# Kernel optimization log

Measured on AMD Instinct MI355X. Metric: run time of the kernel, lower is better.

The kernel has to match this reference:

```python
import jax, jax.numpy as jnp
import numpy as np
from jax import lax

# --- configuration (matches init_kwargs) ---
NY_I = NX_I = 256      # interior model size
PML = 20               # pml width on each edge
DX = 4.0               # grid spacing (m)
DT = 5e-4              # time step (s); CFL: vmax*DT/DX ~ 0.4 < 0.5
NT = 64                # number of time steps
C1, C2 = 9.0 / 8.0, -1.0 / 24.0   # 4th-order staggered FD coefficients


def _shift(p, axis, off, n):
    idx = [slice(None)] * 3
    idx[axis] = slice(2 + off, 2 + off + n)
    return p[tuple(idx)]


def _dfwd(f, axis):
    # forward (half-cell +) staggered derivative, 4th order, zero halo
    pad = [(0, 0)] * 3
    pad[axis] = (2, 2)
    p = jnp.pad(f, pad)
    n = f.shape[axis]
    return (C1 * (_shift(p, axis, 1, n) - _shift(p, axis, 0, n))
            + C2 * (_shift(p, axis, 2, n) - _shift(p, axis, -1, n))) / DX


def _dbwd(f, axis):
    # backward (half-cell -) staggered derivative, 4th order, zero halo
    pad = [(0, 0)] * 3
    pad[axis] = (2, 2)
    p = jnp.pad(f, pad)
    n = f.shape[axis]
    return (C1 * (_shift(p, axis, 0, n) - _shift(p, axis, -1, n))
            + C2 * (_shift(p, axis, 1, n) - _shift(p, axis, -2, n))) / DX


def _propagate(lamb, mu, buoyancy, amps, src_loc, rec_loc):
    # replicate model edges into the PML region (as deepwave does)
    lambp = jnp.pad(lamb, PML, mode='edge')[None]      # [1,NY,NX]
    mup = jnp.pad(mu, PML, mode='edge')[None]
    buoyp = jnp.pad(buoyancy, PML, mode='edge')[None]
    NY, NX = lambp.shape[1], lambp.shape[2]
    n_shots = amps.shape[0]
    l2m = lambp + 2.0 * mup

    # CPML damping profiles (quadratic), alpha=0, kappa=1
    max_vel = lax.stop_gradient(jnp.max(jnp.sqrt(l2m * buoyp)))
    sig_max = 3.0 * max_vel * jnp.log(1000.0) / (2.0 * PML * DX)

    def prof(n):
        i = jnp.arange(n, dtype=lamb.dtype)
        d = jnp.maximum(jnp.clip(PML - i, 0.0, None),
                        jnp.clip(i - (n - 1 - PML), 0.0, None)) / PML
        return sig_max * d * d

    by = jnp.exp(-prof(NY) * DT)[None, :, None]
    ay = by - 1.0
    bx = jnp.exp(-prof(NX) * DT)[None, None, :]
    ax = bx - 1.0

    shot = jnp.arange(n_shots)[:, None]
    sl = src_loc + PML   # [S,nsrc,2]
    rl = rec_loc + PML   # [S,nrec,2]
    src_b = buoyp[0, sl[..., 0], sl[..., 1]]   # buoyancy at sources [S,nsrc]

    z = jnp.zeros((n_shots, NY, NX), lamb.dtype)
    carry0 = (z,) * 13  # vy,vx,syy,sxy,sxx, m_vyy,m_vyx,m_vxy,m_vxx, m_syyy,m_sxyy,m_sxyx,m_sxxx

    def step(carry, amp_t):
        (vy, vx, syy, sxy, sxx,
         mvyy, mvyx, mvxy, mvxx,
         msyyy, msxyy, msxyx, msxxx) = carry
        # --- velocity update ---
        d = _dbwd(syy, 1); msyyy = by * msyyy + ay * d; dsyy_y = d + msyyy
        d = _dbwd(sxy, 2); msxyx = bx * msxyx + ax * d; dsxy_x = d + msxyx
        vy = vy + DT * buoyp * (dsyy_y + dsxy_x)
        d = _dbwd(sxy, 1); msxyy = by * msxyy + ay * d; dsxy_y = d + msxyy
        d = _dbwd(sxx, 2); msxxx = bx * msxxx + ax * d; dsxx_x = d + msxxx
        vx = vx + DT * buoyp * (dsxy_y + dsxx_x)
        # --- inject y-oriented sources into vy ---
        vy = vy.at[shot, sl[..., 0], sl[..., 1]].add(DT * src_b * amp_t)
        # --- stress update ---
        d = _dfwd(vy, 1); mvyy = by * mvyy + ay * d; dvy_y = d + mvyy
        d = _dfwd(vx, 2); mvxx = bx * mvxx + ax * d; dvx_x = d + mvxx
        syy = syy + DT * (l2m * dvy_y + lambp * dvx_x)
        sxx = sxx + DT * (lambp * dvy_y + l2m * dvx_x)
        d = _dfwd(vy, 2); mvyx = bx * mvyx + ax * d; dvy_x = d + mvyx
        d = _dfwd(vx, 1); mvxy = by * mvxy + ay * d; dvx_y = d + mvxy
        sxy = sxy + DT * mup * (dvy_x + dvx_y)
        # --- record y-oriented receivers ---
        rec = vy[shot, rl[..., 0], rl[..., 1]]   # [S,nrec]
        return ((vy, vx, syy, sxy, sxx,
                 mvyy, mvyx, mvxy, mvxx,
                 msyyy, msxyy, msxyx, msxxx), rec)

    _, recs = lax.scan(step, carry0, jnp.moveaxis(amps, 2, 0))  # recs [nt,S,nrec]
    return jnp.transpose(recs, (1, 2, 0))  # [S,nrec,nt]


def setup_inputs() -> dict:
    key = jax.random.key(0)
    k = jax.random.split(key, 6)
    vp = 3000.0 + 100.0 * jax.random.normal(k[0], (NY_I, NX_I), jnp.float32)
    vs = 1500.0 + 50.0 * jax.random.normal(k[1], (NY_I, NX_I), jnp.float32)
    rho = 2200.0 + 50.0 * jax.random.normal(k[2], (NY_I, NX_I), jnp.float32)
    mu = rho * vs ** 2
    lamb = rho * (vp ** 2 - 2.0 * vs ** 2)
    buoyancy = 1.0 / rho
    source_amplitudes_y = jax.random.normal(k[3], (2, 8, NT), jnp.float32)
    source_locations_y = jax.random.randint(k[4], (2, 8, 2), 0, NY_I)
    receiver_locations_y = jax.random.randint(k[5], (2, 64, 2), 0, NY_I)
    return {
        'lamb': lamb, 'mu': mu, 'buoyancy': buoyancy,
        'source_amplitudes_y': source_amplitudes_y,
        'source_locations_y': source_locations_y,
        'receiver_locations_y': receiver_locations_y,
    }


def reference(lamb, mu, buoyancy, source_amplitudes_y,
              source_locations_y, receiver_locations_y):
    return _propagate(lamb, mu, buoyancy, source_amplitudes_y,
                      source_locations_y, receiver_locations_y)
```

## Files before the change

### kernel.cpp

```cpp
#include <hip/hip_runtime.h>
#include <math.h>

static constexpr int NYI  = 256;
static constexpr int PMLW = 20;
static constexpr int NY   = 296, NX = 296;
static constexpr int NCELL = NY * NX;
static constexpr int NS   = 2;
static constexpr int NSRC = 8;
static constexpr int NREC = 64;
static constexpr int NT   = 64;
static constexpr float DXF = 4.0f;
static constexpr float DTF = 5e-4f;
static constexpr float FC1 = 9.0f / 8.0f;
static constexpr float FC2 = -1.0f / 24.0f;
static constexpr float INV_DX = 1.0f / DXF;

static constexpr int TB = 8, TS = 37;
static constexpr int VS = TS + 4;
static constexpr int SS = TS + 8;
static constexpr int NBLK = TB * TB * NS;
static constexpr int NTHR = 512;
static constexpr int VAREA = VS * VS;
static constexpr int TAREA = TS * TS;
static constexpr int SFRAME = SS * SS - TAREA;
static constexpr int KV = 4, KT = 3;

static constexpr int GSLOT   = 3 * NS * NCELL;
static constexpr int FLG_OFF = 2 * GSLOT;

__device__ __forceinline__ float cohload(const float* p) {
    return __hip_atomic_load(p, __ATOMIC_RELAXED, __HIP_MEMORY_SCOPE_AGENT);
}
__device__ __forceinline__ void cohstore(float* p, float v) {
    __hip_atomic_store(p, v, __ATOMIC_RELAXED, __HIP_MEMORY_SCOPE_AGENT);
}

__global__ __launch_bounds__(NTHR, 1)
void elastic_fused(const float* __restrict__ lamb, const float* __restrict__ mu,
                   const float* __restrict__ buoy, const float* __restrict__ amps,
                   const int* __restrict__ src_loc, const int* __restrict__ rec_loc,
                   float* __restrict__ out, float* __restrict__ ws)
{
    __shared__ float sS[3][SS * SS];
    __shared__ float sV[2][VS * VS];
    __shared__ float byt[VS], ayt[VS], bxt[VS], axt[VS];
    __shared__ float sAmp[NSRC * NT];
    __shared__ float wmax[NTHR / 64];
    __shared__ int   rcnt;
    __shared__ short rl_r[NREC];
    __shared__ int   rl_pos[NREC];

    int* flags = (int*)(ws + FLG_OFF);
    float* gstr = ws;

    const int tid  = threadIdx.x;
    const int shot = blockIdx.x & 1;
    const int tb   = blockIdx.x >> 1;
    const int bty  = tb >> 3, btx = tb & 7;
    const int gy0  = bty * TS, gx0 = btx * TS;
    const int myBlk = blockIdx.x;

    int myNbr = -1;
    if (tid < 8) {
        int idx = tid < 4 ? tid : tid + 1;
        int dy = idx / 3 - 1, dx = idx % 3 - 1;
        int nty = bty + dy, ntx = btx + dx;
        if (nty >= 0 && nty < TB && ntx >= 0 && ntx < TB)
            myNbr = ((nty * TB + ntx) << 1) | shot;
    }

    for (int i = tid; i < 3 * SS * SS; i += NTHR) ((float*)sS)[i] = 0.0f;
    for (int i = tid; i < 2 * VS * VS; i += NTHR) ((float*)sV)[i] = 0.0f;
    if (tid == 0) rcnt = 0;

    float vmax = 0.0f;
    for (int i = tid * 4; i < NYI * NYI; i += NTHR * 4) {
        const float4 la4 = *(const float4*)(lamb + i);
        const float4 mu4 = *(const float4*)(mu + i);
        const float4 b4  = *(const float4*)(buoy + i);
        vmax = fmaxf(vmax, (la4.x + 2.0f * mu4.x) * b4.x);
        vmax = fmaxf(vmax, (la4.y + 2.0f * mu4.y) * b4.y);
        vmax = fmaxf(vmax, (la4.z + 2.0f * mu4.z) * b4.z);
        vmax = fmaxf(vmax, (la4.w + 2.0f * mu4.w) * b4.w);
    }
    #pragma unroll
    for (int off = 32; off > 0; off >>= 1)
        vmax = fmaxf(vmax, __shfl_down(vmax, off));
    if ((tid & 63) == 0) wmax[tid >> 6] = vmax;

    int   sidx_v[KV], vyv[KV], vxv[KV], smk[KV];
    float buo_v[KV];
    float msyyy[KV] = {0,0,0,0}, msxyx[KV] = {0,0,0,0};
    float msxyy[KV] = {0,0,0,0}, msxxx[KV] = {0,0,0,0};
    unsigned cvm = 0, intm = 0;
    #pragma unroll
    for (int k = 0; k < KV; ++k) {
        int vi = tid + NTHR * k;
        bool val = vi < VAREA;
        int vy_ = val ? vi / VS : 0;
        int vx_ = val ? vi - vy_ * VS : 0;
        int gy = gy0 - 2 + vy_, gx = gx0 - 2 + vx_;
        bool ing = val && gy >= 0 && gy < NY && gx >= 0 && gx < NX;
        if (ing) cvm |= 1u << k;
        if (ing && vy_ >= 4 && vy_ <= 37 && vx_ >= 4 && vx_ <= 37) intm |= 1u << k;
        vyv[k] = vy_; vxv[k] = vx_;
        sidx_v[k] = (vy_ + 2) * SS + (vx_ + 2);
        float b = 0.0f;
        if (ing) {
            int iy = min(max(gy - PMLW, 0), NYI - 1);
            int ix = min(max(gx - PMLW, 0), NYI - 1);
            b = buoy[iy * NYI + ix];
        }
        buo_v[k] = b;
        int sm = 0;
        #pragma unroll
        for (int s = 0; s < NSRC; ++s) {
            int sy = src_loc[(shot * NSRC + s) * 2 + 0] + PMLW;
            int sx = src_loc[(shot * NSRC + s) * 2 + 1] + PMLW;
            if (ing && sy == gy && sx == gx) sm |= 1 << s;
        }
        smk[k] = sm;
    }
    const unsigned bndm = cvm & ~intm;

    int   sidx_t[KT], vidx_t[KT], gidx_t[KT], tyt[KT], txt[KT];
    float lam_t[KT], mu_t[KT], l2m_t[KT];
    float mvyy[KT] = {0,0,0}, mvxx[KT] = {0,0,0}, mvyx[KT] = {0,0,0}, mvxy[KT] = {0,0,0};
    unsigned ctm = 0, ringm = 0;
    #pragma unroll
    for (int k = 0; k < KT; ++k) {
        int ti = tid + NTHR * k;
        bool val = ti < TAREA;
        int ty = val ? ti / TS : 0;
        int tx = val ? ti - ty * TS : 0;
        int gy = gy0 + ty, gx = gx0 + tx;
        if (val) ctm |= 1u << k;
        if (val && (ty < 4 || ty >= TS - 4 || tx < 4 || tx >= TS - 4)) ringm |= 1u << k;
        tyt[k] = ty; txt[k] = tx;
        sidx_t[k] = (ty + 4) * SS + (tx + 4);
        vidx_t[k] = (ty + 2) * VS + (tx + 2);
        gidx_t[k] = gy * NX + gx;
        float la = 0.0f, m = 0.0f;
        if (val) {
            int iy = min(max(gy - PMLW, 0), NYI - 1);
            int ix = min(max(gx - PMLW, 0), NYI - 1);
            la = lamb[iy * NYI + ix];
            m  = mu  [iy * NYI + ix];
        }
        lam_t[k] = la; mu_t[k] = m; l2m_t[k] = la + 2.0f * m;
    }

    bool fval[2], fin[2];
    int  flidx[2], fgi[2];
    #pragma unroll
    for (int k = 0; k < 2; ++k) {
        int ff = tid + NTHR * k;
        fval[k] = ff < SFRAME;
        int fy = 0, fx = 0;
        if (fval[k]) {
            if (ff < 4 * SS)      { fy = ff / SS;                 fx = ff - fy * SS; }
            else if (ff < 8 * SS) { int r = ff - 4 * SS; fy = SS - 4 + r / SS; fx = r % SS; }
            else {
                int r = ff - 8 * SS;
                if (r < (SS - 8) * 4) { fy = 4 + (r >> 2); fx = r & 3; }
                else { r -= (SS - 8) * 4; fy = 4 + (r >> 2); fx = SS - 4 + (r & 3); }
            }
        }
        int gy = gy0 - 4 + fy, gx = gx0 - 4 + fx;
        fin[k]   = fval[k] && gy >= 0 && gy < NY && gx >= 0 && gx < NX;
        flidx[k] = fy * SS + fx;
        fgi[k]   = fin[k] ? (gy * NX + gx) : 0;
    }

    __syncthreads();

    float vall = wmax[0];
    #pragma unroll
    for (int w = 1; w < NTHR / 64; ++w) vall = fmaxf(vall, wmax[w]);
    const float max_vel = sqrtf(vall);
    const float sig_max = 3.0f * max_vel * logf(1000.0f) / (2.0f * PMLW * DXF);
    if (tid < VS) {
        auto prof = [&](int g) -> float {
            float fi = (float)g;
            float d1 = fmaxf((float)PMLW - fi, 0.0f);
            float d2 = fmaxf(fi - (float)(NY - 1 - PMLW), 0.0f);
            float dd = fmaxf(d1, d2) * (1.0f / (float)PMLW);
            return expf(-(sig_max * dd * dd) * DTF);
        };
        float b = prof(gy0 - 2 + tid); byt[tid] = b; ayt[tid] = b - 1.0f;
        b = prof(gx0 - 2 + tid);       bxt[tid] = b; axt[tid] = b - 1.0f;
    }
    if (tid < NREC) {
        int r = tid;
        int ry = rec_loc[(shot * NREC + r) * 2 + 0] + PMLW;
        int rx = rec_loc[(shot * NREC + r) * 2 + 1] + PMLW;
        if (ry >= gy0 && ry < gy0 + TS && rx >= gx0 && rx < gx0 + TS) {
            int p = atomicAdd(&rcnt, 1);
            rl_r[p]   = (short)r;
            rl_pos[p] = (ry - gy0 + 2) * VS + (rx - gx0 + 2);
        }
    }
    for (int i = tid; i < NSRC * NT; i += NTHR)
        sAmp[i] = amps[shot * NSRC * NT + i];
    __syncthreads();

    auto do_vel = [&](unsigned m, int t) {
        #pragma unroll
        for (int k = 0; k < KV; ++k) {
            if (!((m >> k) & 1)) continue;
            int si = sidx_v[k];
            float by_ = byt[vyv[k]], ay_ = ayt[vyv[k]];
            float bx_ = bxt[vxv[k]], ax_ = axt[vxv[k]];
            float d, mm;
            d = (FC1 * (sS[0][si] - sS[0][si - SS]) + FC2 * (sS[0][si + SS] - sS[0][si - 2 * SS])) * INV_DX;
            mm = by_ * msyyy[k] + ay_ * d;  msyyy[k] = mm;  float dsyy_y = d + mm;
            d = (FC1 * (sS[1][si] - sS[1][si - 1]) + FC2 * (sS[1][si + 1] - sS[1][si - 2])) * INV_DX;
            mm = bx_ * msxyx[k] + ax_ * d;  msxyx[k] = mm;  float dsxy_x = d + mm;
            d = (FC1 * (sS[1][si] - sS[1][si - SS]) + FC2 * (sS[1][si + SS] - sS[1][si - 2 * SS])) * INV_DX;
            mm = by_ * msxyy[k] + ay_ * d;  msxyy[k] = mm;  float dsxy_y = d + mm;
            d = (FC1 * (sS[2][si] - sS[2][si - 1]) + FC2 * (sS[2][si + 1] - sS[2][si - 2])) * INV_DX;
            mm = bx_ * msxxx[k] + ax_ * d;  msxxx[k] = mm;  float dsxx_x = d + mm;
            int vi = tid + NTHR * k;
            float nvy = sV[0][vi] + DTF * buo_v[k] * (dsyy_y + dsxy_x);
            float nvx = sV[1][vi] + DTF * buo_v[k] * (dsxy_y + dsxx_x);
            if (smk[k]) {
                #pragma unroll
                for (int s = 0; s < NSRC; ++s)
                    if ((smk[k] >> s) & 1) nvy += DTF * buo_v[k] * sAmp[s * NT + t];
            }
            sV[0][vi] = nvy;
            sV[1][vi] = nvx;
        }
    };

    for (int t = 0; t < NT; ++t) {
        const float* gsr = gstr + ((t + 1) & 1) * GSLOT;
        float*       gsw = gstr + (t & 1) * GSLOT;

        do_vel(intm, t);

        if (t > 0 && myNbr >= 0) {
            while (__hip_atomic_load(&flags[myNbr], __ATOMIC_RELAXED,
                                     __HIP_MEMORY_SCOPE_AGENT) < t)
                __builtin_amdgcn_s_sleep(1);
        }
        __syncthreads();

        float fr0[3], fr1[3];
        #pragma unroll
        for (int f = 0; f < 3; ++f) {
            fr0[f] = (t > 0 && fin[0]) ? cohload(&gsr[(f * NS + shot) * NCELL + fgi[0]]) : 0.0f;
            fr1[f] = (t > 0 && fin[1]) ? cohload(&gsr[(f * NS + shot) * NCELL + fgi[1]]) : 0.0f;
        }
        if (fval[0]) { sS[0][flidx[0]] = fr0[0]; sS[1][flidx[0]] = fr0[1]; sS[2][flidx[0]] = fr0[2]; }
        if (fval[1]) { sS[0][flidx[1]] = fr1[0]; sS[1][flidx[1]] = fr1[1]; sS[2][flidx[1]] = fr1[2]; }
        __syncthreads();

        do_vel(bndm, t);
        __syncthreads();

        if (tid < rcnt)
            out[(shot * NREC + rl_r[tid]) * NT + t] = sV[0][rl_pos[tid]];

        #pragma unroll
        for (int k = 0; k < KT; ++k) {
            if (!((ctm >> k) & 1)) continue;
            int si = sidx_t[k], vi = vidx_t[k];
            float by_ = byt[tyt[k] + 2], ay_ = ayt[tyt[k] + 2];
            float bx_ = bxt[txt[k] + 2], ax_ = axt[txt[k] + 2];
            float d, mm;
            d = (FC1 * (sV[0][vi + VS] - sV[0][vi]) + FC2 * (sV[0][vi + 2 * VS] - sV[0][vi - VS])) * INV_DX;
            mm = by_ * mvyy[k] + ay_ * d;  mvyy[k] = mm;  float dvy_y = d + mm;
            d = (FC1 * (sV[1][vi + 1] - sV[1][vi]) + FC2 * (sV[1][vi + 2] - sV[1][vi - 1])) * INV_DX;
            mm = bx_ * mvxx[k] + ax_ * d;  mvxx[k] = mm;  float dvx_x = d + mm;
            float nsyy = sS[0][si] + DTF * (l2m_t[k] * dvy_y + lam_t[k] * dvx_x);
            float nsxx = sS[2][si] + DTF * (lam_t[k] * dvy_y + l2m_t[k] * dvx_x);
            d = (FC1 * (sV[0][vi + 1] - sV[0][vi]) + FC2 * (sV[0][vi + 2] - sV[0][vi - 1])) * INV_DX;
            mm = bx_ * mvyx[k] + ax_ * d;  mvyx[k] = mm;  float dvy_x = d + mm;
            d = (FC1 * (sV[1][vi + VS] - sV[1][vi]) + FC2 * (sV[1][vi + 2 * VS] - sV[1][vi - VS])) * INV_DX;
            mm = by_ * mvxy[k] + ay_ * d;  mvxy[k] = mm;  float dvx_y = d + mm;
            float nsxy = sS[1][si] + DTF * mu_t[k] * (dvy_x + dvx_y);
            sS[0][si] = nsyy; sS[1][si] = nsxy; sS[2][si] = nsxx;
            if ((ringm >> k) & 1) {
                int gi = gidx_t[k];
                cohstore(&gsw[(0 * NS + shot) * NCELL + gi], nsyy);
                cohstore(&gsw[(1 * NS + shot) * NCELL + gi], nsxy);
                cohstore(&gsw[(2 * NS + shot) * NCELL + gi], nsxx);
            }
        }

        __syncthreads();
        if (tid == 0 && t < NT - 1)
            __hip_atomic_store(&flags[myBlk], t + 1, __ATOMIC_RELAXED,
                               __HIP_MEMORY_SCOPE_AGENT);
    }
}

extern "C" void kernel_launch(void* const* d_in, const int* in_sizes, int n_in,
                              void* d_out, int out_size, void* d_ws, size_t ws_size,
                              hipStream_t stream) {
    const float* lamb    = (const float*)d_in[0];
    const float* mu      = (const float*)d_in[1];
    const float* buoy    = (const float*)d_in[2];
    const float* amps    = (const float*)d_in[3];
    const int*   src_loc = (const int*)d_in[4];
    const int*   rec_loc = (const int*)d_in[5];
    float* ws  = (float*)d_ws;
    float* out = (float*)d_out;

    hipMemsetAsync(ws + FLG_OFF, 0, NBLK * sizeof(int), stream);

    elastic_fused<<<NBLK, NTHR, 0, stream>>>(lamb, mu, buoy, amps, src_loc, rec_loc, out, ws);
}
```

Measured before the change: 341.3 us.

## Register-block 4 cells per thread with padded LDS rows and vector accesses

Reorganizes the fused elastic time-stepping kernel so each thread owns a horizontal run of 4 cells for both velocity and stress updates. The thread keeps its own field values in registers rather than re-reading them from LDS, and reads neighbours with float4/float2 LDS loads. LDS rows are padded to a 48-float stride so these vector accesses stay aligned. The aim is fewer LDS instructions and less per-thread index overhead, at the cost of more registers per thread and a less even split of boundary versus interior work across threads.

```diff
diff --git a/kernel.cpp b/kernel.cpp
--- a/kernel.cpp
+++ b/kernel.cpp
@@ -20,10 +20,13 @@
 static constexpr int SS = TS + 8;
 static constexpr int NBLK = TB * TB * NS;
 static constexpr int NTHR = 512;
-static constexpr int VAREA = VS * VS;
 static constexpr int TAREA = TS * TS;
 static constexpr int SFRAME = SS * SS - TAREA;
-static constexpr int KV = 4, KT = 3;
+static constexpr int LDP   = 48;
+static constexpr int NVRUN = 11;
+static constexpr int NTRUN = 10;
+static constexpr int NVT   = VS * NVRUN;
+static constexpr int NST   = TS * NTRUN;
 
 static constexpr int GSLOT   = 3 * NS * NCELL;
 static constexpr int FLG_OFF = 2 * GSLOT;
@@ -41,9 +44,9 @@
                    const int* __restrict__ src_loc, const int* __restrict__ rec_loc,
                    float* __restrict__ out, float* __restrict__ ws)
 {
-    __shared__ float sS[3][SS * SS];
-    __shared__ float sV[2][VS * VS];
-    __shared__ float byt[VS], ayt[VS], bxt[VS], axt[VS];
+    __shared__ float4 sS4[3][SS * (LDP / 4)];
+    __shared__ float4 sV4[2][VS * (LDP / 4)];
+    __shared__ __align__(16) float byt[44], ayt[44], bxt[44], axt[44];
     __shared__ float sAmp[NSRC * NT];
     __shared__ float wmax[NTHR / 64];
     __shared__ int   rcnt;
@@ -59,6 +62,12 @@
     const int bty  = tb >> 3, btx = tb & 7;
     const int gy0  = bty * TS, gx0 = btx * TS;
     const int myBlk = blockIdx.x;
+
+    float* S0f = (float*)sS4[0];
+    float* S1f = (float*)sS4[1];
+    float* S2f = (float*)sS4[2];
+    float* V0f = (float*)sV4[0];
+    float* V1f = (float*)sV4[1];
 
     int myNbr = -1;
     if (tid < 8) {
@@ -69,8 +78,8 @@
             myNbr = ((nty * TB + ntx) << 1) | shot;
     }
 
-    for (int i = tid; i < 3 * SS * SS; i += NTHR) ((float*)sS)[i] = 0.0f;
-    for (int i = tid; i < 2 * VS * VS; i += NTHR) ((float*)sV)[i] = 0.0f;
+    for (int i = tid; i < 3 * SS * (LDP / 4); i += NTHR) ((float4*)sS4)[i] = make_float4(0, 0, 0, 0);
+    for (int i = tid; i < 2 * VS * (LDP / 4); i += NTHR) ((float4*)sV4)[i] = make_float4(0, 0, 0, 0);
     if (tid == 0) rcnt = 0;
 
     float vmax = 0.0f;
@@ -88,66 +97,60 @@
         vmax = fmaxf(vmax, __shfl_down(vmax, off));
     if ((tid & 63) == 0) wmax[tid >> 6] = vmax;
 
-    int   sidx_v[KV], vyv[KV], vxv[KV], smk[KV];
-    float buo_v[KV];
-    float msyyy[KV] = {0,0,0,0}, msxyx[KV] = {0,0,0,0};
-    float msxyy[KV] = {0,0,0,0}, msxxx[KV] = {0,0,0,0};
-    unsigned cvm = 0, intm = 0;
-    #pragma unroll
-    for (int k = 0; k < KV; ++k) {
-        int vi = tid + NTHR * k;
-        bool val = vi < VAREA;
-        int vy_ = val ? vi / VS : 0;
-        int vx_ = val ? vi - vy_ * VS : 0;
-        int gy = gy0 - 2 + vy_, gx = gx0 - 2 + vx_;
-        bool ing = val && gy >= 0 && gy < NY && gx >= 0 && gx < NX;
-        if (ing) cvm |= 1u << k;
-        if (ing && vy_ >= 4 && vy_ <= 37 && vx_ >= 4 && vx_ <= 37) intm |= 1u << k;
-        vyv[k] = vy_; vxv[k] = vx_;
-        sidx_v[k] = (vy_ + 2) * SS + (vx_ + 2);
-        float b = 0.0f;
-        if (ing) {
-            int iy = min(max(gy - PMLW, 0), NYI - 1);
-            int ix = min(max(gx - PMLW, 0), NYI - 1);
-            b = buoy[iy * NYI + ix];
-        }
-        buo_v[k] = b;
-        int sm = 0;
-        #pragma unroll
-        for (int s = 0; s < NSRC; ++s) {
-            int sy = src_loc[(shot * NSRC + s) * 2 + 0] + PMLW;
-            int sx = src_loc[(shot * NSRC + s) * 2 + 1] + PMLW;
-            if (ing && sy == gy && sx == gx) sm |= 1 << s;
-        }
-        smk[k] = sm;
-    }
-    const unsigned bndm = cvm & ~intm;
-
-    int   sidx_t[KT], vidx_t[KT], gidx_t[KT], tyt[KT], txt[KT];
-    float lam_t[KT], mu_t[KT], l2m_t[KT];
-    float mvyy[KT] = {0,0,0}, mvxx[KT] = {0,0,0}, mvyx[KT] = {0,0,0}, mvxy[KT] = {0,0,0};
-    unsigned ctm = 0, ringm = 0;
-    #pragma unroll
-    for (int k = 0; k < KT; ++k) {
-        int ti = tid + NTHR * k;
-        bool val = ti < TAREA;
-        int ty = val ? ti / TS : 0;
-        int tx = val ? ti - ty * TS : 0;
-        int gy = gy0 + ty, gx = gx0 + tx;
-        if (val) ctm |= 1u << k;
-        if (val && (ty < 4 || ty >= TS - 4 || tx < 4 || tx >= TS - 4)) ringm |= 1u << k;
-        tyt[k] = ty; txt[k] = tx;
-        sidx_t[k] = (ty + 4) * SS + (tx + 4);
-        vidx_t[k] = (ty + 2) * VS + (tx + 2);
-        gidx_t[k] = gy * NX + gx;
-        float la = 0.0f, m = 0.0f;
-        if (val) {
-            int iy = min(max(gy - PMLW, 0), NYI - 1);
-            int ix = min(max(gx - PMLW, 0), NYI - 1);
-            la = lamb[iy * NYI + ix];
-            m  = mu  [iy * NYI + ix];
-        }
-        lam_t[k] = la; mu_t[k] = m; l2m_t[k] = la + 2.0f * m;
+    const bool vthr = tid < NVT;
+    int vy_ = 0, vx0 = 0;
+    bool vint = false;
+    unsigned vmask = 0;
+    float buo4[4] = {0, 0, 0, 0};
+    int   smk4[4] = {0, 0, 0, 0};
+    float m_syyy[4] = {0,0,0,0}, m_sxyx[4] = {0,0,0,0}, m_sxyy[4] = {0,0,0,0}, m_sxxx[4] = {0,0,0,0};
+    float rvy[4] = {0,0,0,0}, rvx[4] = {0,0,0,0};
+    if (vthr) {
+        vy_ = tid / NVRUN; vx0 = (tid - vy_ * NVRUN) * 4;
+        int gy = gy0 - 2 + vy_;
+        bool rowok = gy >= 0 && gy < NY;
+        #pragma unroll
+        for (int j = 0; j < 4; ++j) {
+            int vx_ = vx0 + j, gx = gx0 - 2 + vx_;
+            bool ok = rowok && vx_ < VS && gx >= 0 && gx < NX;
+            if (ok) {
+                vmask |= 1u << j;
+                int iy = min(max(gy - PMLW, 0), NYI - 1);
+                int ix = min(max(gx - PMLW, 0), NYI - 1);
+                buo4[j] = buoy[iy * NYI + ix];
+                #pragma unroll
+                for (int s = 0; s < NSRC; ++s) {
+                    int sy = src_loc[(shot * NSRC + s) * 2 + 0] + PMLW;
+                    int sx = src_loc[(shot * NSRC + s) * 2 + 1] + PMLW;
+                    if (sy == gy && sx == gx) smk4[j] |= 1 << s;
+                }
+            }
+        }
+        vint = (vy_ >= 4 && vy_ <= 37 && vx0 >= 4 && vx0 + 3 <= 37);
+    }
+
+    const bool sthr = tid < NST;
+    int ty = 0, tx0 = 0, gbase = 0;
+    unsigned tmask = 0, rmask = 0;
+    float lam4[4] = {0,0,0,0}, mu4a[4] = {0,0,0,0}, l2m4[4] = {0,0,0,0};
+    float m_vyy[4] = {0,0,0,0}, m_vxx[4] = {0,0,0,0}, m_vyx[4] = {0,0,0,0}, m_vxy[4] = {0,0,0,0};
+    float rsyy[4] = {0,0,0,0}, rsxy[4] = {0,0,0,0}, rsxx[4] = {0,0,0,0};
+    if (sthr) {
+        ty = tid / NTRUN; tx0 = (tid - ty * NTRUN) * 4;
+        gbase = (gy0 + ty) * NX + gx0 + tx0;
+        #pragma unroll
+        for (int j = 0; j < 4; ++j) {
+            int tx = tx0 + j;
+            if (tx < TS) {
+                tmask |= 1u << j;
+                if (ty < 4 || ty >= TS - 4 || tx < 4 || tx >= TS - 4) rmask |= 1u << j;
+                int gy = gy0 + ty, gx = gx0 + tx;
+                int iy = min(max(gy - PMLW, 0), NYI - 1);
+                int ix = min(max(gx - PMLW, 0), NYI - 1);
+                float la = lamb[iy * NYI + ix], m = mu[iy * NYI + ix];
+                lam4[j] = la; mu4a[j] = m; l2m4[j] = la + 2.0f * m;
+            }
+        }
     }
 
     bool fval[2], fin[2];
@@ -168,7 +171,7 @@
         }
         int gy = gy0 - 4 + fy, gx = gx0 - 4 + fx;
         fin[k]   = fval[k] && gy >= 0 && gy < NY && gx >= 0 && gx < NX;
-        flidx[k] = fy * SS + fx;
+        flidx[k] = fy * LDP + fx;
         fgi[k]   = fin[k] ? (gy * NX + gx) : 0;
     }
 
@@ -179,7 +182,7 @@
     for (int w = 1; w < NTHR / 64; ++w) vall = fmaxf(vall, wmax[w]);
     const float max_vel = sqrtf(vall);
     const float sig_max = 3.0f * max_vel * logf(1000.0f) / (2.0f * PMLW * DXF);
-    if (tid < VS) {
+    if (tid < 44) {
         auto prof = [&](int g) -> float {
             float fi = (float)g;
             float d1 = fmaxf((float)PMLW - fi, 0.0f);
@@ -197,47 +200,143 @@
         if (ry >= gy0 && ry < gy0 + TS && rx >= gx0 && rx < gx0 + TS) {
             int p = atomicAdd(&rcnt, 1);
             rl_r[p]   = (short)r;
-            rl_pos[p] = (ry - gy0 + 2) * VS + (rx - gx0 + 2);
+            rl_pos[p] = (ry - gy0 + 2) * LDP + (rx - gx0 + 2);
         }
     }
     for (int i = tid; i < NSRC * NT; i += NTHR)
         sAmp[i] = amps[shot * NSRC * NT + i];
     __syncthreads();
 
-    auto do_vel = [&](unsigned m, int t) {
-        #pragma unroll
-        for (int k = 0; k < KV; ++k) {
-            if (!((m >> k) & 1)) continue;
-            int si = sidx_v[k];
-            float by_ = byt[vyv[k]], ay_ = ayt[vyv[k]];
-            float bx_ = bxt[vxv[k]], ax_ = axt[vxv[k]];
+    float byv = 0, ayv = 0, bxa[4] = {0,0,0,0}, axa[4] = {0,0,0,0};
+    if (vthr) {
+        byv = byt[vy_]; ayv = ayt[vy_];
+        const float4 b4 = *(const float4*)&bxt[vx0];
+        const float4 a4 = *(const float4*)&axt[vx0];
+        bxa[0] = b4.x; bxa[1] = b4.y; bxa[2] = b4.z; bxa[3] = b4.w;
+        axa[0] = a4.x; axa[1] = a4.y; axa[2] = a4.z; axa[3] = a4.w;
+    }
+    float byS = 0, ayS = 0, bxS[4] = {0,0,0,0}, axS[4] = {0,0,0,0};
+    if (sthr) {
+        byS = byt[ty + 2]; ayS = ayt[ty + 2];
+        #pragma unroll
+        for (int j = 0; j < 4; ++j) { bxS[j] = bxt[tx0 + 2 + j]; axS[j] = axt[tx0 + 2 + j]; }
+    }
+
+    auto vel_body = [&](int t) {
+        const int rb2 = (vy_ + 2) * LDP + vx0;
+        const float4 A = *(const float4*)(S1f + rb2);
+        const float4 B = *(const float4*)(S1f + rb2 + 4);
+        const float4 C = *(const float4*)(S2f + rb2);
+        const float4 D = *(const float4*)(S2f + rb2 + 4);
+        const float a8[8] = {A.x, A.y, A.z, A.w, B.x, B.y, B.z, B.w};
+        const float c8[8] = {C.x, C.y, C.z, C.w, D.x, D.y, D.z, D.w};
+        float sy0[4], sy1[4], sy2[4], sy3[4];
+        float xy0[4], xy1[4], xy3[4];
+        {
+            const int cb = vx0 + 2;
+            float2 p, q;
+            p = *(const float2*)(S0f + (vy_ + 0) * LDP + cb); q = *(const float2*)(S0f + (vy_ + 0) * LDP + cb + 2);
+            sy0[0] = p.x; sy0[1] = p.y; sy0[2] = q.x; sy0[3] = q.y;
+            p = *(const float2*)(S0f + (vy_ + 1) * LDP + cb); q = *(const float2*)(S0f + (vy_ + 1) * LDP + cb + 2);
+            sy1[0] = p.x; sy1[1] = p.y; sy1[2] = q.x; sy1[3] = q.y;
+            p = *(const float2*)(S0f + (vy_ + 2) * LDP + cb); q = *(const float2*)(S0f + (vy_ + 2) * LDP + cb + 2);
+            sy2[0] = p.x; sy2[1] = p.y; sy2[2] = q.x; sy2[3] = q.y;
+            p = *(const float2*)(S0f + (vy_ + 3) * LDP + cb); q = *(const float2*)(S0f + (vy_ + 3) * LDP + cb + 2);
+            sy3[0] = p.x; sy3[1] = p.y; sy3[2] = q.x; sy3[3] = q.y;
+            p = *(const float2*)(S1f + (vy_ + 0) * LDP + cb); q = *(const float2*)(S1f + (vy_ + 0) * LDP + cb + 2);
+            xy0[0] = p.x; xy0[1] = p.y; xy0[2] = q.x; xy0[3] = q.y;
+            p = *(const float2*)(S1f + (vy_ + 1) * LDP + cb); q = *(const float2*)(S1f + (vy_ + 1) * LDP + cb + 2);
+            xy1[0] = p.x; xy1[1] = p.y; xy1[2] = q.x; xy1[3] = q.y;
+            p = *(const float2*)(S1f + (vy_ + 3) * LDP + cb); q = *(const float2*)(S1f + (vy_ + 3) * LDP + cb + 2);
+            xy3[0] = p.x; xy3[1] = p.y; xy3[2] = q.x; xy3[3] = q.y;
+        }
+        #pragma unroll
+        for (int j = 0; j < 4; ++j) {
+            float nvy = 0.0f, nvx = 0.0f;
+            if (vmask & (1u << j)) {
+                float d, mm;
+                d = (FC1 * (sy2[j] - sy1[j]) + FC2 * (sy3[j] - sy0[j])) * INV_DX;
+                mm = byv * m_syyy[j] + ayv * d;  m_syyy[j] = mm;  float dsyy_y = d + mm;
+                d = (FC1 * (a8[j + 2] - a8[j + 1]) + FC2 * (a8[j + 3] - a8[j])) * INV_DX;
+                mm = bxa[j] * m_sxyx[j] + axa[j] * d;  m_sxyx[j] = mm;  float dsxy_x = d + mm;
+                nvy = rvy[j] + DTF * buo4[j] * (dsyy_y + dsxy_x);
+                d = (FC1 * (a8[j + 2] - xy1[j]) + FC2 * (xy3[j] - xy0[j])) * INV_DX;
+                mm = byv * m_sxyy[j] + ayv * d;  m_sxyy[j] = mm;  float dsxy_y = d + mm;
+                d = (FC1 * (c8[j + 2] - c8[j + 1]) + FC2 * (c8[j + 3] - c8[j])) * INV_DX;
+                mm = bxa[j] * m_sxxx[j] + axa[j] * d;  m_sxxx[j] = mm;  float dsxx_x = d + mm;
+                nvx = rvx[j] + DTF * buo4[j] * (dsxy_y + dsxx_x);
+                if (smk4[j]) {
+                    #pragma unroll
+                    for (int s = 0; s < NSRC; ++s)
+                        if ((smk4[j] >> s) & 1) nvy += DTF * buo4[j] * sAmp[s * NT + t];
+                }
+            }
+            rvy[j] = nvy; rvx[j] = nvx;
+        }
+        *(float4*)(V0f + vy_ * LDP + vx0) = make_float4(rvy[0], rvy[1], rvy[2], rvy[3]);
+        *(float4*)(V1f + vy_ * LDP + vx0) = make_float4(rvx[0], rvx[1], rvx[2], rvx[3]);
+    };
+
+    auto str_body = [&](int t, float* gsw) {
+        const int rb2 = (ty + 2) * LDP + tx0;
+        const float4 A = *(const float4*)(V0f + rb2);
+        const float4 B = *(const float4*)(V0f + rb2 + 4);
+        const float4 C = *(const float4*)(V1f + rb2);
+        const float4 D = *(const float4*)(V1f + rb2 + 4);
+        const float a8[8] = {A.x, A.y, A.z, A.w, B.x, B.y, B.z, B.w};
+        const float c8[8] = {C.x, C.y, C.z, C.w, D.x, D.y, D.z, D.w};
+        float vyr0[4], vyr2[4], vyr3[4];
+        float vxr0[4], vxr2[4], vxr3[4];
+        {
+            const int cb = tx0 + 2;
+            float2 p, q;
+            p = *(const float2*)(V0f + (ty + 1) * LDP + cb); q = *(const float2*)(V0f + (ty + 1) * LDP + cb + 2);
+            vyr0[0] = p.x; vyr0[1] = p.y; vyr0[2] = q.x; vyr0[3] = q.y;
+            p = *(const float2*)(V0f + (ty + 3) * LDP + cb); q = *(const float2*)(V0f + (ty + 3) * LDP + cb + 2);
+            vyr2[0] = p.x; vyr2[1] = p.y; vyr2[2] = q.x; vyr2[3] = q.y;
+            p = *(const float2*)(V0f + (ty + 4) * LDP + cb); q = *(const float2*)(V0f + (ty + 4) * LDP + cb + 2);
+            vyr3[0] = p.x; vyr3[1] = p.y; vyr3[2] = q.x; vyr3[3] = q.y;
+            p = *(const float2*)(V1f + (ty + 1) * LDP + cb); q = *(const float2*)(V1f + (ty + 1) * LDP + cb + 2);
+            vxr0[0] = p.x; vxr0[1] = p.y; vxr0[2] = q.x; vxr0[3] = q.y;
+            p = *(const float2*)(V1f + (ty + 3) * LDP + cb); q = *(const float2*)(V1f + (ty + 3) * LDP + cb + 2);
+            vxr2[0] = p.x; vxr2[1] = p.y; vxr2[2] = q.x; vxr2[3] = q.y;
+            p = *(const float2*)(V1f + (ty + 4) * LDP + cb); q = *(const float2*)(V1f + (ty + 4) * LDP + cb + 2);
+            vxr3[0] = p.x; vxr3[1] = p.y; vxr3[2] = q.x; vxr3[3] = q.y;
+        }
+        #pragma unroll
+        for (int j = 0; j < 4; ++j) {
+            if (!(tmask & (1u << j))) continue;
             float d, mm;
-            d = (FC1 * (sS[0][si] - sS[0][si - SS]) + FC2 * (sS[0][si + SS] - sS[0][si - 2 * SS])) * INV_DX;
-            mm = by_ * msyyy[k] + ay_ * d;  msyyy[k] = mm;  float dsyy_y = d + mm;
-            d = (FC1 * (sS[1][si] - sS[1][si - 1]) + FC2 * (sS[1][si + 1] - sS[1][si - 2])) * INV_DX;
-            mm = bx_ * msxyx[k] + ax_ * d;  msxyx[k] = mm;  float dsxy_x = d + mm;
-            d = (FC1 * (sS[1][si] - sS[1][si - SS]) + FC2 * (sS[1][si + SS] - sS[1][si - 2 * SS])) * INV_DX;
-            mm = by_ * msxyy[k] + ay_ * d;  msxyy[k] = mm;  float dsxy_y = d + mm;
-            d = (FC1 * (sS[2][si] - sS[2][si - 1]) + FC2 * (sS[2][si + 1] - sS[2][si - 2])) * INV_DX;
-            mm = bx_ * msxxx[k] + ax_ * d;  msxxx[k] = mm;  float dsxx_x = d + mm;
-            int vi = tid + NTHR * k;
-            float nvy = sV[0][vi] + DTF * buo_v[k] * (dsyy_y + dsxy_x);
-            float nvx = sV[1][vi] + DTF * buo_v[k] * (dsxy_y + dsxx_x);
-            if (smk[k]) {
-                #pragma unroll
-                for (int s = 0; s < NSRC; ++s)
-                    if ((smk[k] >> s) & 1) nvy += DTF * buo_v[k] * sAmp[s * NT + t];
-            }
-            sV[0][vi] = nvy;
-            sV[1][vi] = nvx;
-        }
+            d = (FC1 * (vyr2[j] - a8[j + 2]) + FC2 * (vyr3[j] - vyr0[j])) * INV_DX;
+            mm = byS * m_vyy[j] + ayS * d;  m_vyy[j] = mm;  float dvy_y = d + mm;
+            d = (FC1 * (c8[j + 3] - c8[j + 2]) + FC2 * (c8[j + 4] - c8[j + 1])) * INV_DX;
+            mm = bxS[j] * m_vxx[j] + axS[j] * d;  m_vxx[j] = mm;  float dvx_x = d + mm;
+            float nsyy = rsyy[j] + DTF * (l2m4[j] * dvy_y + lam4[j] * dvx_x);
+            float nsxx = rsxx[j] + DTF * (lam4[j] * dvy_y + l2m4[j] * dvx_x);
+            d = (FC1 * (a8[j + 3] - a8[j + 2]) + FC2 * (a8[j + 4] - a8[j + 1])) * INV_DX;
+            mm = bxS[j] * m_vyx[j] + axS[j] * d;  m_vyx[j] = mm;  float dvy_x = d + mm;
+            d = (FC1 * (vxr2[j] - c8[j + 2]) + FC2 * (vxr3[j] - vxr0[j])) * INV_DX;
+            mm = byS * m_vxy[j] + ayS * d;  m_vxy[j] = mm;  float dvx_y = d + mm;
+            float nsxy = rsxy[j] + DTF * mu4a[j] * (dvy_x + dvx_y);
+            rsyy[j] = nsyy; rsxy[j] = nsxy; rsxx[j] = nsxx;
+            if (rmask & (1u << j)) {
+                int gi = gbase + j;
+                cohstore(&gsw[(0 * NS + shot) * NCELL + gi], nsyy);
+                cohstore(&gsw[(1 * NS + shot) * NCELL + gi], nsxy);
+                cohstore(&gsw[(2 * NS + shot) * NCELL + gi], nsxx);
+            }
+        }
+        const int so = (ty + 4) * LDP + tx0 + 4;
+        *(float4*)(S0f + so) = make_float4(rsyy[0], rsyy[1], rsyy[2], rsyy[3]);
+        *(float4*)(S1f + so) = make_float4(rsxy[0], rsxy[1], rsxy[2], rsxy[3]);
+        *(float4*)(S2f + so) = make_float4(rsxx[0], rsxx[1], rsxx[2], rsxx[3]);
     };
 
     for (int t = 0; t < NT; ++t) {
         const float* gsr = gstr + ((t + 1) & 1) * GSLOT;
         float*       gsw = gstr + (t & 1) * GSLOT;
 
-        do_vel(intm, t);
+        if (vthr && vint) vel_body(t);
 
         if (t > 0 && myNbr >= 0) {
             while (__hip_atomic_load(&flags[myNbr], __ATOMIC_RELAXED,
@@ -252,42 +351,17 @@
             fr0[f] = (t > 0 && fin[0]) ? cohload(&gsr[(f * NS + shot) * NCELL + fgi[0]]) : 0.0f;
             fr1[f] = (t > 0 && fin[1]) ? cohload(&gsr[(f * NS + shot) * NCELL + fgi[1]]) : 0.0f;
         }
-        if (fval[0]) { sS[0][flidx[0]] = fr0[0]; sS[1][flidx[0]] = fr0[1]; sS[2][flidx[0]] = fr0[2]; }
-        if (fval[1]) { sS[0][flidx[1]] = fr1[0]; sS[1][flidx[1]] = fr1[1]; sS[2][flidx[1]] = fr1[2]; }
+        if (fval[0]) { S0f[flidx[0]] = fr0[0]; S1f[flidx[0]] = fr0[1]; S2f[flidx[0]] = fr0[2]; }
+        if (fval[1]) { S0f[flidx[1]] = fr1[0]; S1f[flidx[1]] = fr1[1]; S2f[flidx[1]] = fr1[2]; }
         __syncthreads();
 
-        do_vel(bndm, t);
+        if (vthr && !vint) vel_body(t);
         __syncthreads();
 
         if (tid < rcnt)
-            out[(shot * NREC + rl_r[tid]) * NT + t] = sV[0][rl_pos[tid]];
-
-        #pragma unroll
-        for (int k = 0; k < KT; ++k) {
-            if (!((ctm >> k) & 1)) continue;
-            int si = sidx_t[k], vi = vidx_t[k];
-            float by_ = byt[tyt[k] + 2], ay_ = ayt[tyt[k] + 2];
-            float bx_ = bxt[txt[k] + 2], ax_ = axt[txt[k] + 2];
-            float d, mm;
-            d = (FC1 * (sV[0][vi + VS] - sV[0][vi]) + FC2 * (sV[0][vi + 2 * VS] - sV[0][vi - VS])) * INV_DX;
-            mm = by_ * mvyy[k] + ay_ * d;  mvyy[k] = mm;  float dvy_y = d + mm;
-            d = (FC1 * (sV[1][vi + 1] - sV[1][vi]) + FC2 * (sV[1][vi + 2] - sV[1][vi - 1])) * INV_DX;
-            mm = bx_ * mvxx[k] + ax_ * d;  mvxx[k] = mm;  float dvx_x = d + mm;
-            float nsyy = sS[0][si] + DTF * (l2m_t[k] * dvy_y + lam_t[k] * dvx_x);
-            float nsxx = sS[2][si] + DTF * (lam_t[k] * dvy_y + l2m_t[k] * dvx_x);
-            d = (FC1 * (sV[0][vi + 1] - sV[0][vi]) + FC2 * (sV[0][vi + 2] - sV[0][vi - 1])) * INV_DX;
-            mm = bx_ * mvyx[k] + ax_ * d;  mvyx[k] = mm;  float dvy_x = d + mm;
-            d = (FC1 * (sV[1][vi + VS] - sV[1][vi]) + FC2 * (sV[1][vi + 2 * VS] - sV[1][vi - VS])) * INV_DX;
-            mm = by_ * mvxy[k] + ay_ * d;  mvxy[k] = mm;  float dvx_y = d + mm;
-            float nsxy = sS[1][si] + DTF * mu_t[k] * (dvy_x + dvx_y);
-            sS[0][si] = nsyy; sS[1][si] = nsxy; sS[2][si] = nsxx;
-            if ((ringm >> k) & 1) {
-                int gi = gidx_t[k];
-                cohstore(&gsw[(0 * NS + shot) * NCELL + gi], nsyy);
-                cohstore(&gsw[(1 * NS + shot) * NCELL + gi], nsxy);
-                cohstore(&gsw[(2 * NS + shot) * NCELL + gi], nsxx);
-            }
-        }
+            out[(shot * NREC + rl_r[tid]) * NT + t] = V0f[rl_pos[tid]];
+
+        if (sthr) str_body(t, gsw);
 
         __syncthreads();
         if (tid == 0 && t < NT - 1)
```

Result: slower. 454.8 us (+33.3%).
